# Optimization experiments

Hardware: AMD Instinct MI355X
Metric: run time of the kernel (lower is better)

The kernel has to match this reference:

```python
import jax, jax.numpy as jnp
import numpy as np

N = 3072          # n_vertices
D = 512           # embedding_size (hardcoded in module)
ALPHA = 0.2       # LeakyReLU slope
AVG_DEG = 32
NEG_INF = -9e15
N_ITERS = 10
TRIPLET_MARGIN = 400.0


def setup_inputs() -> dict:
    key = jax.random.key(0)
    ks = jax.random.split(key, 14)
    s = 0.05  # weight init scale
    emb = jax.random.normal(ks[0], (N, D), dtype=jnp.float32) * 0.1
    # symmetric 0/1 adjacency, no self loops, density ~ AVG_DEG/N
    u = jax.random.uniform(ks[1], (N, N))
    A = jnp.triu((u < (AVG_DEG / N)).astype(jnp.float32), 1)
    adj = A + A.T
    rn = lambda k, shp: jax.random.normal(k, shp, dtype=jnp.float32) * s
    return {
        "embeddings": emb,
        "adj": adj,
        "W_n": rn(ks[2], (D, D)), "a_src_n": rn(ks[3], (D,)), "a_dst_n": rn(ks[4], (D,)),
        "W_nn": rn(ks[5], (D, D)), "a_src_nn": rn(ks[6], (D,)), "a_dst_nn": rn(ks[7], (D,)),
        "W_u": rn(ks[8], (2 * D, D)), "b_u": jnp.zeros((D,), dtype=jnp.float32),
        "W_g": rn(ks[9], (D, D)), "a_src_g": rn(ks[10], (D,)), "a_dst_g": rn(ks[11], (D,)),
    }


def _gat_attention(h, adj, W, a_src, a_dst):
    # standard pyGAT layer: Wh = hW; e_ij = LeakyReLU(a_src.Wh_i + a_dst.Wh_j)
    Wh = h @ W                                   # [N, D]
    e = jax.nn.leaky_relu((Wh @ a_src)[:, None] + (Wh @ a_dst)[None, :], ALPHA)
    att = jax.nn.softmax(jnp.where(adj > 0, e, NEG_INF), axis=1)  # [N, N]
    return att, Wh


def reference(embeddings, adj, W_n, a_src_n, a_dst_n, W_nn, a_src_nn, a_dst_nn,
              W_u, b_u, W_g, a_src_g, a_dst_g):
    n = embeddings.shape[0]
    inv_adj = 1.0 - adj - jnp.eye(n, dtype=adj.dtype)  # non-neighbors, no self
    emb = embeddings
    for _ in range(N_ITERS):
        att_n, Wh_n = _gat_attention(emb, adj, W_n, a_src_n, a_dst_n)
        neigh = jax.nn.elu(att_n @ Wh_n)               # concat=True -> ELU
        att_nn, Wh_nn = _gat_attention(emb, inv_adj, W_nn, a_src_nn, a_dst_nn)
        non_neigh = jax.nn.elu(att_nn @ Wh_nn)
        cat = jnp.concatenate([neigh, non_neigh], axis=1)  # [N, 2D]
        emb = jax.nn.relu(emb + cat @ W_u + b_u)
    sq = jnp.sum(emb * emb, axis=1)
    d2 = sq[:, None] + sq[None, :] - 2.0 * (emb @ emb.T)
    dist = jnp.sqrt(jnp.maximum(d2, 1e-12))            # [N, N]
    embedding_loss = jnp.sum(dist * (-adj))
    triplet_loss = jnp.maximum(embedding_loss + TRIPLET_MARGIN, 0.0)
    # glimpse layer returns the attention matrix itself
    att_g, _ = _gat_attention(emb, adj, W_g, a_src_g, a_dst_g)
    confidence = jnp.max(att_g, axis=1)
    log_conf = jnp.mean(jnp.log(confidence + 1e-8) - jnp.log(1e-8))
    return jnp.stack([triplet_loss, embedding_loss, log_conf])
```

## Files before the change

### kernel.cpp

```cpp
#include <hip/hip_runtime.h>
#include <math.h>

#define N_V 3072
#define D_E 512
#define EDGE_CAP 128
constexpr float LRELU_ALPHA = 0.2f;
constexpr float NEG_INF_F = -9e15f;

typedef __attribute__((ext_vector_type(8))) short bf16x8;
typedef __attribute__((ext_vector_type(4))) float f32x4;
typedef __attribute__((ext_vector_type(4))) unsigned short ushort4v;
typedef __attribute__((ext_vector_type(2))) unsigned short ushort2v;

__device__ inline unsigned short f2bf(float f) {
    union { float f; unsigned int u; } x; x.f = f;
    unsigned int r = x.u + 0x7fffu + ((x.u >> 16) & 1u);
    return (unsigned short)(r >> 16);
}
__device__ inline float bf2f(unsigned short b) {
    union { unsigned int u; float f; } x; x.u = ((unsigned int)b) << 16;
    return x.f;
}

__device__ inline void xcd_swizzle(int& bx, int& by) {
    int gx = gridDim.x, nwg = gx * gridDim.y;
    int flat = by * gx + bx;
    int q = nwg >> 3;
    int swz = (flat & 7) * q + (flat >> 3);
    bx = swz % gx; by = swz / gx;
}

template<int EPI>
__global__ __launch_bounds__(256) void gemm_bf16(
    const unsigned short* __restrict__ A,
    const unsigned short* __restrict__ BT,
    int M, int N, int K,
    unsigned short* __restrict__ C0, int ldc0,
    unsigned short* __restrict__ C1,
    const float* __restrict__ addv,
    const float* __restrict__ bias,
    float* __restrict__ Cf)
{
    constexpr int BM = 128, BN = 64, BK = 64;
    __shared__ unsigned short As[BM * BK + BN * BK];
    unsigned short* Bs = As + BM * BK;
    const int tid  = threadIdx.x;
    int bxi = blockIdx.x, byi = blockIdx.y;
    xcd_swizzle(bxi, byi);
    const int bm   = byi * BM, bn = bxi * BN;
    const int lane = tid & 63, wid = tid >> 6;
    const int wr   = wid >> 1, wc = wid & 1;
    const int lr   = lane & 15, lk = lane >> 4;

    f32x4 acc[4][2];
    #pragma unroll
    for (int i = 0; i < 4; ++i)
        #pragma unroll
        for (int j = 0; j < 2; ++j)
            acc[i][j] = (f32x4)(0.f);

    auto asp = (__attribute__((address_space(3))) unsigned short*)As;
    auto bsp = (__attribute__((address_space(3))) unsigned short*)Bs;

    for (int k0 = 0; k0 < K; k0 += BK) {
        #pragma unroll
        for (int l = 0; l < 4; ++l) {
            int li = l * 256 + tid;
            int row = li >> 3, slot = li & 7;
            int gs = slot ^ (row & 7);
            __builtin_amdgcn_global_load_lds(
                (const __attribute__((address_space(1))) void*)(A + (size_t)(bm + row) * K + k0 + gs * 8),
                (__attribute__((address_space(3))) void*)(asp + li * 8), 16, 0, 0);
        }
        #pragma unroll
        for (int l = 0; l < 2; ++l) {
            int li = l * 256 + tid;
            int row = li >> 3, slot = li & 7;
            int gs = slot ^ (row & 7);
            __builtin_amdgcn_global_load_lds(
                (const __attribute__((address_space(1))) void*)(BT + (size_t)(bn + row) * K + k0 + gs * 8),
                (__attribute__((address_space(3))) void*)(bsp + li * 8), 16, 0, 0);
        }
        __syncthreads();

        #pragma unroll
        for (int ks = 0; ks < 2; ++ks) {
            bf16x8 af[4], bfr[2];
            #pragma unroll
            for (int fm = 0; fm < 4; ++fm) {
                int row = wr * 64 + fm * 16 + lr;
                int sl = (ks * 4 + lk) ^ (row & 7);
                af[fm] = *(const bf16x8*)(As + row * BK + sl * 8);
            }
            #pragma unroll
            for (int fn = 0; fn < 2; ++fn) {
                int col = wc * 32 + fn * 16 + lr;
                int sl = (ks * 4 + lk) ^ (col & 7);
                bfr[fn] = *(const bf16x8*)(Bs + col * BK + sl * 8);
            }
            #pragma unroll
            for (int fm = 0; fm < 4; ++fm)
                #pragma unroll
                for (int fn = 0; fn < 2; ++fn)
                    acc[fm][fn] = __builtin_amdgcn_mfma_f32_16x16x32_bf16(
                        af[fm], bfr[fn], acc[fm][fn], 0, 0, 0);
        }
        __syncthreads();
    }

    if (EPI == 2) {
        #pragma unroll
        for (int fm = 0; fm < 4; ++fm) {
            #pragma unroll
            for (int fn = 0; fn < 2; ++fn) {
                int row0 = bm + wr * 64 + fm * 16 + lk * 4;
                int col  = bn + wc * 32 + fn * 16 + lr;
                f32x4 v = acc[fm][fn];
                #pragma unroll
                for (int r = 0; r < 4; ++r) {
                    float x = v[r] + addv[(size_t)(row0 + r) * N + col] + bias[col];
                    x = x > 0.f ? x : 0.f;
                    Cf[(size_t)(row0 + r) * N + col] = x;
                    C0[(size_t)(row0 + r) * ldc0 + col] = f2bf(x);
                }
            }
        }
    } else {
        if (bn < 512) {
            #pragma unroll
            for (int fm = 0; fm < 4; ++fm) {
                #pragma unroll
                for (int fn = 0; fn < 2; ++fn) {
                    int row0 = bm + wr * 64 + fm * 16 + lk * 4;
                    int col  = bn + wc * 32 + fn * 16 + lr;
                    #pragma unroll
                    for (int r = 0; r < 4; ++r)
                        C0[(size_t)(row0 + r) * ldc0 + col] = f2bf(acc[fm][fn][r]);
                }
            }
        } else if (bn < 1024) {
            constexpr int TS = 136;
            unsigned short* Ts = As;
            #pragma unroll
            for (int fm = 0; fm < 4; ++fm) {
                #pragma unroll
                for (int fn = 0; fn < 2; ++fn) {
                    int rloc = wr * 64 + fm * 16 + lk * 4;
                    int lc   = wc * 32 + fn * 16 + lr;
                    ushort4v pk;
                    pk.x = f2bf(acc[fm][fn][0]); pk.y = f2bf(acc[fm][fn][1]);
                    pk.z = f2bf(acc[fm][fn][2]); pk.w = f2bf(acc[fm][fn][3]);
                    *(ushort4v*)(Ts + lc * TS + rloc) = pk;
                }
            }
            __syncthreads();
            for (int idx = tid; idx < 64 * 16; idx += 256) {
                int c = idx >> 4, seg = idx & 15;
                bf16x8 pk = *(const bf16x8*)(Ts + c * TS + seg * 8);
                *(bf16x8*)(C1 + (size_t)(bn - 512 + c) * M + bm + seg * 8) = pk;
            }
        } else {
            #pragma unroll
            for (int fm = 0; fm < 4; ++fm) {
                #pragma unroll
                for (int fn = 0; fn < 2; ++fn) {
                    int row0 = bm + wr * 64 + fm * 16 + lk * 4;
                    int col  = bn + wc * 32 + fn * 16 + lr;
                    if (col >= 1024 && col < 1030) {
                        int v = col - 1024;
                        #pragma unroll
                        for (int r = 0; r < 4; ++r)
                            Cf[(size_t)v * N_V + row0 + r] = acc[fm][fn][r];
                    }
                }
            }
        }
    }
}

__global__ __launch_bounds__(256) void gemm_nn64(
    const unsigned short* __restrict__ A,
    const unsigned short* __restrict__ BT,
    unsigned short* __restrict__ cat)
{
    constexpr int BM = 64, BN = 64, BK = 64, K = N_V;
    __shared__ unsigned short As[BM * BK];
    __shared__ unsigned short Bs[BN * BK];
    const int tid = threadIdx.x;
    int bxi = blockIdx.x, byi = blockIdx.y;
    xcd_swizzle(bxi, byi);
    const int bm = byi * BM, bn = bxi * BN;
    const int lane = tid & 63, wid = tid >> 6;
    const int wr = wid >> 1, wc = wid & 1;
    const int lr = lane & 15, lk = lane >> 4;

    f32x4 acc[2][2];
    #pragma unroll
    for (int i = 0; i < 2; ++i)
        #pragma unroll
        for (int j = 0; j < 2; ++j)
            acc[i][j] = (f32x4)(0.f);

    auto asp = (__attribute__((address_space(3))) unsigned short*)As;
    auto bsp = (__attribute__((address_space(3))) unsigned short*)Bs;

    for (int k0 = 0; k0 < K; k0 += BK) {
        #pragma unroll
        for (int l = 0; l < 2; ++l) {
            int li = l * 256 + tid;
            int row = li >> 3, slot = li & 7;
            int gs = slot ^ (row & 7);
            __builtin_amdgcn_global_load_lds(
                (const __attribute__((address_space(1))) void*)(A + (size_t)(bm + row) * K + k0 + gs * 8),
                (__attribute__((address_space(3))) void*)(asp + li * 8), 16, 0, 0);
        }
        #pragma unroll
        for (int l = 0; l < 2; ++l) {
            int li = l * 256 + tid;
            int row = li >> 3, slot = li & 7;
            int gs = slot ^ (row & 7);
            __builtin_amdgcn_global_load_lds(
                (const __attribute__((address_space(1))) void*)(BT + (size_t)(bn + row) * K + k0 + gs * 8),
                (__attribute__((address_space(3))) void*)(bsp + li * 8), 16, 0, 0);
        }
        __syncthreads();

        #pragma unroll
        for (int ks = 0; ks < 2; ++ks) {
            bf16x8 af[2], bfr[2];
            #pragma unroll
            for (int fm = 0; fm < 2; ++fm) {
                int row = wr * 32 + fm * 16 + lr;
                int sl = (ks * 4 + lk) ^ (row & 7);
                af[fm] = *(const bf16x8*)(As + row * BK + sl * 8);
            }
            #pragma unroll
            for (int fn = 0; fn < 2; ++fn) {
                int col = wc * 32 + fn * 16 + lr;
                int sl = (ks * 4 + lk) ^ (col & 7);
                bfr[fn] = *(const bf16x8*)(Bs + col * BK + sl * 8);
            }
            #pragma unroll
            for (int fm = 0; fm < 2; ++fm)
                #pragma unroll
                for (int fn = 0; fn < 2; ++fn)
                    acc[fm][fn] = __builtin_amdgcn_mfma_f32_16x16x32_bf16(
                        af[fm], bfr[fn], acc[fm][fn], 0, 0, 0);
        }
        __syncthreads();
    }

    #pragma unroll
    for (int fm = 0; fm < 2; ++fm) {
        #pragma unroll
        for (int fn = 0; fn < 2; ++fn) {
            int row0 = bm + wr * 32 + fm * 16 + lk * 4;
            int col  = bn + wc * 32 + fn * 16 + lr;
            #pragma unroll
            for (int r = 0; r < 4; ++r) {
                float x = acc[fm][fn][r];
                x = x > 0.f ? x : (expf(x) - 1.f);
                cat[(size_t)(row0 + r) * (2 * D_E) + D_E + col] = f2bf(x);
            }
        }
    }
}

__global__ __launch_bounds__(256) void convT_f32_bf16(
    const float* __restrict__ W, unsigned short* __restrict__ WT, int K, int Nw)
{
    int k = blockIdx.x * 256 + threadIdx.x;
    int n = blockIdx.y;
    if (k < K) WT[(size_t)n * K + k] = f2bf(W[(size_t)k * Nw + n]);
}

__global__ __launch_bounds__(256) void conv_bf16(
    const float* __restrict__ X, unsigned short* __restrict__ Y, int n)
{
    int i = blockIdx.x * 256 + threadIdx.x;
    if (i < n) Y[i] = f2bf(X[i]);
}

__global__ __launch_bounds__(256) void conv_wv_rows(
    const float* __restrict__ wv, unsigned short* __restrict__ W2Tx)
{
    int k = threadIdx.x + (blockIdx.x & 1) * 256;
    int v = blockIdx.x >> 1;
    W2Tx[(size_t)(1024 + v) * D_E + k] = f2bf(wv[v * D_E + k]);
}

__global__ __launch_bounds__(256) void build_graph(
    const float* __restrict__ adj, int* __restrict__ edges,
    int* __restrict__ deg, unsigned int* __restrict__ bitmask)
{
    const int i = blockIdx.x, t = threadIdx.x;
    __shared__ int cnts[256];
    unsigned int word = 0;
    int c = 0;
    if (t < 96) {
        #pragma unroll
        for (int b = 0; b < 32; ++b) {
            int j = t * 32 + b;
            if (adj[(size_t)i * N_V + j] > 0.f) { word |= (1u << b); ++c; }
        }
    }
    cnts[t] = c;
    __syncthreads();
    for (int o = 1; o < 256; o <<= 1) {
        int add = (t >= o) ? cnts[t - o] : 0;
        __syncthreads();
        cnts[t] += add;
        __syncthreads();
    }
    int base = cnts[t] - c;
    if (t < 96) {
        int k = 0;
        #pragma unroll
        for (int b = 0; b < 32; ++b) {
            if ((word >> b) & 1u) {
                int pos = base + k;
                if (pos < EDGE_CAP) edges[(size_t)i * EDGE_CAP + pos] = t * 32 + b;
                ++k;
            }
        }
        bitmask[(size_t)i * 96 + t] = word;
    }
    if (t == 0) deg[i] = cnts[255] < EDGE_CAP ? cnts[255] : EDGE_CAP;
}

__global__ __launch_bounds__(256) void matvec6(
    const float* __restrict__ W_n, const float* __restrict__ W_nn,
    const float* __restrict__ W_g,
    const float* __restrict__ as_n, const float* __restrict__ ad_n,
    const float* __restrict__ as_nn, const float* __restrict__ ad_nn,
    const float* __restrict__ as_g, const float* __restrict__ ad_g,
    float* __restrict__ wv)
{
    const int wave = threadIdx.x >> 6, lane = threadIdx.x & 63;
    const int r = blockIdx.x * 4 + wave;
    float a0 = 0, a1 = 0, a2 = 0, a3 = 0, a4 = 0, a5 = 0;
    #pragma unroll
    for (int k = 0; k < 8; ++k) {
        int c = lane + k * 64;
        float wn = W_n[(size_t)r * D_E + c];
        float wm = W_nn[(size_t)r * D_E + c];
        float wg = W_g[(size_t)r * D_E + c];
        a0 = fmaf(wn, as_n[c], a0);  a1 = fmaf(wn, ad_n[c], a1);
        a2 = fmaf(wm, as_nn[c], a2); a3 = fmaf(wm, ad_nn[c], a3);
        a4 = fmaf(wg, as_g[c], a4);  a5 = fmaf(wg, ad_g[c], a5);
    }
    #pragma unroll
    for (int off = 32; off; off >>= 1) {
        a0 += __shfl_down(a0, off); a1 += __shfl_down(a1, off);
        a2 += __shfl_down(a2, off); a3 += __shfl_down(a3, off);
        a4 += __shfl_down(a4, off); a5 += __shfl_down(a5, off);
    }
    if (lane == 0) {
        wv[0 * D_E + r] = a0; wv[1 * D_E + r] = a1;
        wv[2 * D_E + r] = a2; wv[3 * D_E + r] = a3;
        wv[4 * D_E + r] = a4; wv[5 * D_E + r] = a5;
    }
}

template<int NV>
__global__ __launch_bounds__(256) void sd_dots(
    const unsigned short* __restrict__ emb, const float* __restrict__ wv,
    float* __restrict__ outs)
{
    const int wave = threadIdx.x >> 6, lane = threadIdx.x & 63;
    const int i = blockIdx.x * 4 + wave;
    float acc[NV];
    #pragma unroll
    for (int v = 0; v < NV; ++v) acc[v] = 0.f;
    #pragma unroll
    for (int k = 0; k < 8; ++k) {
        int c = lane + k * 64;
        float x = bf2f(emb[(size_t)i * D_E + c]);
        #pragma unroll
        for (int v = 0; v < NV; ++v) acc[v] = fmaf(x, wv[v * D_E + c], acc[v]);
    }
    #pragma unroll
    for (int off = 32; off; off >>= 1)
        #pragma unroll
        for (int v = 0; v < NV; ++v) acc[v] += __shfl_down(acc[v], off);
    if (lane == 0)
        #pragma unroll
        for (int v = 0; v < NV; ++v) outs[v * N_V + i] = acc[v];
}

__global__ __launch_bounds__(256) void nn_sm_gather(
    const unsigned int* __restrict__ bitmask,
    const int* __restrict__ edges, const int* __restrict__ deg,
    const float* __restrict__ sd,
    const unsigned short* __restrict__ Whn,
    unsigned short* __restrict__ att, unsigned short* __restrict__ cat)
{
    const int t = threadIdx.x;
    __shared__ float red[256];
    if (blockIdx.x < N_V) {
        const int i = blockIdx.x;
        const float* s = sd + 2 * N_V;
        const float* dvec = sd + 3 * N_V;
        __shared__ unsigned int mrow[96];
        if (t < 96) mrow[t] = bitmask[(size_t)i * 96 + t];
        __syncthreads();
        const float si = s[i];
        const float4* dv4 = (const float4*)dvec;
        float e[3][4];
        float mloc = -3.4e38f;
        #pragma unroll
        for (int l = 0; l < 3; ++l) {
            int jv = t + l * 256;
            float4 d = dv4[jv];
            int j0 = jv * 4;
            unsigned int w = mrow[j0 >> 5];
            #pragma unroll
            for (int c = 0; c < 4; ++c) {
                int j = j0 + c;
                bool keep = (((w >> (j & 31)) & 1u) == 0u) && (j != i);
                float x = si + ((const float*)&d)[c];
                x = x > 0.f ? x : LRELU_ALPHA * x;
                e[l][c] = keep ? x : NEG_INF_F;
                mloc = fmaxf(mloc, e[l][c]);
            }
        }
        red[t] = mloc; __syncthreads();
        for (int o = 128; o; o >>= 1) {
            if (t < o) red[t] = fmaxf(red[t], red[t + o]);
            __syncthreads();
        }
        float m = red[0]; __syncthreads();
        float zloc = 0.f;
        #pragma unroll
        for (int l = 0; l < 3; ++l)
            #pragma unroll
            for (int c = 0; c < 4; ++c) { e[l][c] = expf(e[l][c] - m); zloc += e[l][c]; }
        red[t] = zloc; __syncthreads();
        for (int o = 128; o; o >>= 1) {
            if (t < o) red[t] += red[t + o];
            __syncthreads();
        }
        const float zinv = 1.f / red[0];
        #pragma unroll
        for (int l = 0; l < 3; ++l) {
            int jv = t + l * 256;
            ushort4v p;
            p.x = f2bf(e[l][0] * zinv); p.y = f2bf(e[l][1] * zinv);
            p.z = f2bf(e[l][2] * zinv); p.w = f2bf(e[l][3] * zinv);
            *(ushort4v*)(att + (size_t)i * N_V + (size_t)jv * 4) = p;
        }
    } else {
        const int i = blockIdx.x - N_V;
        const float* s = sd;
        const float* dvec = sd + N_V;
        const int cnt = deg[i];
        __shared__ float p[EDGE_CAP];
        __shared__ int lst[EDGE_CAP];
        float ev = -3.4e38f;
        if (t < cnt) {
            int j = edges[(size_t)i * EDGE_CAP + t];
            lst[t] = j;
            float x = s[i] + dvec[j];
            x = x > 0.f ? x : LRELU_ALPHA * x;
            p[t] = x;
            ev = x;
        }
        red[t] = ev; __syncthreads();
        for (int o = 128; o; o >>= 1) {
            if (t < o) red[t] = fmaxf(red[t], red[t + o]);
            __syncthreads();
        }
        float m = red[0]; __syncthreads();
        float pe = 0.f;
        if (t < cnt) { pe = expf(p[t] - m); p[t] = pe; }
        red[t] = pe; __syncthreads();
        for (int o = 128; o; o >>= 1) {
            if (t < o) red[t] += red[t + o];
            __syncthreads();
        }
        const float zinv = 1.f / red[0];
        float a0 = 0.f, a1 = 0.f;
        for (int e = 0; e < cnt; ++e) {
            int j = lst[e];
            float w = p[e] * zinv;
            ushort2v h = *(const ushort2v*)(Whn + (size_t)j * D_E + t * 2);
            a0 = fmaf(w, bf2f(h.x), a0);
            a1 = fmaf(w, bf2f(h.y), a1);
        }
        a0 = a0 > 0.f ? a0 : (expf(a0) - 1.f);
        a1 = a1 > 0.f ? a1 : (expf(a1) - 1.f);
        ushort2v o2; o2.x = f2bf(a0); o2.y = f2bf(a1);
        *(ushort2v*)(cat + (size_t)i * (2 * D_E) + t * 2) = o2;
    }
}

__global__ __launch_bounds__(256) void colsum(
    const float* __restrict__ emb, float* __restrict__ musum)
{
    const int b = blockIdx.x, t = threadIdx.x;
    float s0 = 0.f, s1 = 0.f;
    for (int r = 0; r < 64; ++r) {
        const float* row = emb + (size_t)(b * 64 + r) * D_E;
        s0 += row[t];
        s1 += row[t + 256];
    }
    atomicAdd(&musum[t], s0);
    atomicAdd(&musum[t + 256], s1);
}

__global__ __launch_bounds__(256) void center_bf16(
    const float* __restrict__ emb, const float* __restrict__ musum,
    unsigned short* __restrict__ embc)
{
    int i = blockIdx.x * 256 + threadIdx.x;
    int c = i & (D_E - 1);
    embc[i] = f2bf(emb[i] - musum[c] * (1.f / N_V));
}

__global__ __launch_bounds__(256) void edge_loss_c(
    const int* __restrict__ edges, const int* __restrict__ deg,
    const unsigned short* __restrict__ embc, float* __restrict__ epart)
{
    __shared__ unsigned short rowi[D_E];
    __shared__ float gsum[16];
    const int i = blockIdx.x, t = threadIdx.x;
    if (t < 64) ((bf16x8*)rowi)[t] = ((const bf16x8*)(embc + (size_t)i * D_E))[t];
    __syncthreads();
    const int g = t >> 4, l = t & 15;
    const int cnt = deg[i];
    float sum = 0.f;
    for (int e = g; e < cnt; e += 16) {
        int j = edges[(size_t)i * EDGE_CAP + e];
        float d2 = 0.f;
        #pragma unroll
        for (int q = 0; q < 4; ++q) {
            int off = q * 128 + l * 8;
            bf16x8 a = *(const bf16x8*)(rowi + off);
            bf16x8 b = *(const bf16x8*)(embc + (size_t)j * D_E + off);
            #pragma unroll
            for (int k = 0; k < 8; ++k) {
                float df = bf2f(((unsigned short*)&a)[k]) -
                           bf2f(((unsigned short*)&b)[k]);
                d2 = fmaf(df, df, d2);
            }
        }
        #pragma unroll
        for (int msk = 1; msk < 16; msk <<= 1) d2 += __shfl_xor(d2, msk);
        if (l == 0) sum += sqrtf(fmaxf(d2, 1e-12f));
    }
    if (l == 0) gsum[g] = sum;
    __syncthreads();
    if (t == 0) {
        float tot = 0.f;
        #pragma unroll
        for (int k = 0; k < 16; ++k) tot += gsum[k];
        epart[i] = tot;
    }
}

__global__ __launch_bounds__(256) void conf_kernel(
    const unsigned int* __restrict__ bitmask, const float* __restrict__ s,
    const float* __restrict__ dvec, float* __restrict__ cpart)
{
    const int i = blockIdx.x, t = threadIdx.x;
    __shared__ unsigned int mrow[96];
    __shared__ float red[256];
    if (t < 96) mrow[t] = bitmask[(size_t)i * 96 + t];
    __syncthreads();
    const float si = s[i];
    const float4* dv4 = (const float4*)dvec;
    float e[3][4];
    float mloc = -3.4e38f;
    #pragma unroll
    for (int l = 0; l < 3; ++l) {
        int jv = t + l * 256;
        float4 d = dv4[jv];
        int j0 = jv * 4;
        unsigned int w = mrow[j0 >> 5];
        #pragma unroll
        for (int c = 0; c < 4; ++c) {
            int j = j0 + c;
            bool keep = ((w >> (j & 31)) & 1u) != 0u;
            float x = si + ((const float*)&d)[c];
            x = x > 0.f ? x : LRELU_ALPHA * x;
            e[l][c] = keep ? x : NEG_INF_F;
            mloc = fmaxf(mloc, e[l][c]);
        }
    }
    red[t] = mloc; __syncthreads();
    for (int o = 128; o; o >>= 1) {
        if (t < o) red[t] = fmaxf(red[t], red[t + o]);
        __syncthreads();
    }
    float m = red[0]; __syncthreads();
    float zloc = 0.f;
    #pragma unroll
    for (int l = 0; l < 3; ++l)
        #pragma unroll
        for (int c = 0; c < 4; ++c) zloc += expf(e[l][c] - m);
    red[t] = zloc; __syncthreads();
    for (int o = 128; o; o >>= 1) {
        if (t < o) red[t] += red[t + o];
        __syncthreads();
    }
    if (t == 0) cpart[i] = logf(1.f / red[0] + 1e-8f);
}

__global__ __launch_bounds__(256) void finalize2(
    const float* __restrict__ epart, const float* __restrict__ cpart,
    float* __restrict__ out)
{
    const int t = threadIdx.x;
    float e = 0.f, c = 0.f;
    #pragma unroll
    for (int k = 0; k < 12; ++k) {
        e += epart[t + k * 256];
        c += cpart[t + k * 256];
    }
    __shared__ float re[256], rc[256];
    re[t] = e; rc[t] = c;
    __syncthreads();
    for (int o = 128; o; o >>= 1) {
        if (t < o) { re[t] += re[t + o]; rc[t] += rc[t + o]; }
        __syncthreads();
    }
    if (t == 0) {
        float loss = -re[0];
        out[0] = fmaxf(loss + 400.f, 0.f);
        out[1] = loss;
        out[2] = rc[0] / (float)N_V - logf(1e-8f);
    }
}

extern "C" void kernel_launch(void* const* d_in, const int* in_sizes, int n_in,
                              void* d_out, int out_size, void* d_ws, size_t ws_size,
                              hipStream_t stream) {
    const float* emb_in   = (const float*)d_in[0];
    const float* adj      = (const float*)d_in[1];
    const float* W_n      = (const float*)d_in[2];
    const float* a_src_n  = (const float*)d_in[3];
    const float* a_dst_n  = (const float*)d_in[4];
    const float* W_nn     = (const float*)d_in[5];
    const float* a_src_nn = (const float*)d_in[6];
    const float* a_dst_nn = (const float*)d_in[7];
    const float* W_u      = (const float*)d_in[8];
    const float* b_u      = (const float*)d_in[9];
    const float* W_g      = (const float*)d_in[10];
    const float* a_src_g  = (const float*)d_in[11];
    const float* a_dst_g  = (const float*)d_in[12];
    float* out = (float*)d_out;

    char* p = (char*)d_ws;
    auto alloc = [&](size_t bytes) { char* r = p; p += (bytes + 255) & ~(size_t)255; return r; };

    unsigned short* att_nn  = (unsigned short*)alloc((size_t)N_V * N_V * 2);
    unsigned short* Whn     = (unsigned short*)alloc((size_t)N_V * D_E * 2);
    unsigned short* WhTnn   = (unsigned short*)alloc((size_t)D_E * N_V * 2);
    unsigned short* cat_bf  = (unsigned short*)alloc((size_t)N_V * 2 * D_E * 2);
    float*          embf[2] = { (float*)alloc((size_t)N_V * D_E * 4),
                                (float*)alloc((size_t)N_V * D_E * 4) };
    unsigned short* embb[2] = { (unsigned short*)alloc((size_t)N_V * D_E * 2),
                                (unsigned short*)alloc((size_t)N_V * D_E * 2) };
    unsigned short* embc    = (unsigned short*)alloc((size_t)N_V * D_E * 2);
    unsigned short* W2Tx    = (unsigned short*)alloc((size_t)1088 * D_E * 2);
    unsigned short* WuT     = (unsigned short*)alloc((size_t)D_E * (2 * D_E) * 2);
    float*          wv      = (float*)alloc(6 * D_E * 4);
    float*          sd      = (float*)alloc(6 * N_V * 4);
    float*          sdg     = (float*)alloc(2 * N_V * 4);
    float*          musum   = (float*)alloc(D_E * 4);
    float*          epart   = (float*)alloc(N_V * 4);
    float*          cpart   = (float*)alloc(N_V * 4);
    int*            edges   = (int*)alloc((size_t)N_V * EDGE_CAP * 4);
    int*            deg     = (int*)alloc(N_V * 4);
    unsigned int*   bitmask = (unsigned int*)alloc((size_t)N_V * 96 * 4);

    dim3 blk(256);

    hipMemsetAsync(W2Tx, 0, (size_t)1088 * D_E * 2, stream);
    convT_f32_bf16<<<dim3(2, D_E), blk, 0, stream>>>(W_n, W2Tx, D_E, D_E);
    convT_f32_bf16<<<dim3(2, D_E), blk, 0, stream>>>(W_nn, W2Tx + (size_t)D_E * D_E, D_E, D_E);
    convT_f32_bf16<<<dim3(4, D_E), blk, 0, stream>>>(W_u, WuT, 2 * D_E, D_E);
    conv_bf16<<<(N_V * D_E) / 256, blk, 0, stream>>>(emb_in, embb[0], N_V * D_E);
    hipMemcpyAsync(embf[0], emb_in, (size_t)N_V * D_E * 4, hipMemcpyDeviceToDevice, stream);
    hipMemsetAsync(musum, 0, D_E * sizeof(float), stream);
    build_graph<<<N_V, blk, 0, stream>>>(adj, edges, deg, bitmask);
    matvec6<<<D_E / 4, blk, 0, stream>>>(W_n, W_nn, W_g, a_src_n, a_dst_n,
                                         a_src_nn, a_dst_nn, a_src_g, a_dst_g, wv);
    conv_wv_rows<<<12, blk, 0, stream>>>(wv, W2Tx);

    dim3 gW2(17, N_V / 128);
    dim3 gG(8, N_V / 128);
    dim3 gNN(D_E / 64, N_V / 64);

    int cur = 0;
    for (int it = 0; it < 10; ++it) {
        int nxt = cur ^ 1;
        gemm_bf16<5><<<gW2, blk, 0, stream>>>(embb[cur], W2Tx, N_V, 1088, D_E,
                                              Whn, D_E, WhTnn, nullptr, nullptr, sd);
        nn_sm_gather<<<2 * N_V, blk, 0, stream>>>(bitmask, edges, deg, sd,
                                                  Whn, att_nn, cat_bf);
        gemm_nn64<<<gNN, blk, 0, stream>>>(att_nn, WhTnn, cat_bf);
        gemm_bf16<2><<<gG, blk, 0, stream>>>(cat_bf, WuT, N_V, D_E, 2 * D_E,
                                             embb[nxt], D_E, nullptr, embf[cur], b_u, embf[nxt]);
        cur = nxt;
    }

    colsum<<<N_V / 64, blk, 0, stream>>>(embf[cur], musum);
    center_bf16<<<(N_V * D_E) / 256, blk, 0, stream>>>(embf[cur], musum, embc);
    edge_loss_c<<<N_V, blk, 0, stream>>>(edges, deg, embc, epart);
    sd_dots<2><<<N_V / 4, blk, 0, stream>>>(embb[cur], wv + 4 * D_E, sdg);
    conf_kernel<<<N_V, blk, 0, stream>>>(bitmask, sdg, sdg + N_V, cpart);

    finalize2<<<1, blk, 0, stream>>>(epart, cpart, out);
}
```

Before: 853.8 us.

## Split-K the dense non-neighbor attention GEMM and use edge-list confidence softmax

The non-neighbor attention GEMM (3072x512, K=3072) now uses 128x64 tiles and splits K into two halves across a z-dimension. Each half writes fp32 partials, and a new elementwise kernel sums them, applies ELU and stores bf16 into the concat buffer. This keeps the same block count while giving each block more MFMA work per loaded B tile. The cost is extra fp32 partial traffic and one more launch per iteration. Separately, the glimpse confidence softmax now runs one wave per row over the sparse edge list instead of a dense 3072-wide masked row, which removes most of that kernel's work.

```diff
diff --git a/kernel.cpp b/kernel.cpp
--- a/kernel.cpp
+++ b/kernel.cpp
@@ -178,25 +178,27 @@
     }
 }
 
-__global__ __launch_bounds__(256) void gemm_nn64(
+__global__ __launch_bounds__(256) void gemm_nn_sk(
     const unsigned short* __restrict__ A,
     const unsigned short* __restrict__ BT,
-    unsigned short* __restrict__ cat)
-{
-    constexpr int BM = 64, BN = 64, BK = 64, K = N_V;
+    float* __restrict__ Cp)
+{
+    constexpr int BM = 128, BN = 64, BK = 64, K = N_V;
     __shared__ unsigned short As[BM * BK];
     __shared__ unsigned short Bs[BN * BK];
-    const int tid = threadIdx.x;
+    const int tid  = threadIdx.x;
     int bxi = blockIdx.x, byi = blockIdx.y;
     xcd_swizzle(bxi, byi);
-    const int bm = byi * BM, bn = bxi * BN;
+    const int bm   = byi * BM, bn = bxi * BN;
+    const int kh   = K >> 1;
+    const int kbeg = blockIdx.z * kh, kend = kbeg + kh;
     const int lane = tid & 63, wid = tid >> 6;
-    const int wr = wid >> 1, wc = wid & 1;
-    const int lr = lane & 15, lk = lane >> 4;
-
-    f32x4 acc[2][2];
-    #pragma unroll
-    for (int i = 0; i < 2; ++i)
+    const int wr   = wid >> 1, wc = wid & 1;
+    const int lr   = lane & 15, lk = lane >> 4;
+
+    f32x4 acc[4][2];
+    #pragma unroll
+    for (int i = 0; i < 4; ++i)
         #pragma unroll
         for (int j = 0; j < 2; ++j)
             acc[i][j] = (f32x4)(0.f);
@@ -204,9 +206,9 @@
     auto asp = (__attribute__((address_space(3))) unsigned short*)As;
     auto bsp = (__attribute__((address_space(3))) unsigned short*)Bs;
 
-    for (int k0 = 0; k0 < K; k0 += BK) {
-        #pragma unroll
-        for (int l = 0; l < 2; ++l) {
+    for (int k0 = kbeg; k0 < kend; k0 += BK) {
+        #pragma unroll
+        for (int l = 0; l < 4; ++l) {
             int li = l * 256 + tid;
             int row = li >> 3, slot = li & 7;
             int gs = slot ^ (row & 7);
@@ -227,10 +229,10 @@
 
         #pragma unroll
         for (int ks = 0; ks < 2; ++ks) {
-            bf16x8 af[2], bfr[2];
-            #pragma unroll
-            for (int fm = 0; fm < 2; ++fm) {
-                int row = wr * 32 + fm * 16 + lr;
+            bf16x8 af[4], bfr[2];
+            #pragma unroll
+            for (int fm = 0; fm < 4; ++fm) {
+                int row = wr * 64 + fm * 16 + lr;
                 int sl = (ks * 4 + lk) ^ (row & 7);
                 af[fm] = *(const bf16x8*)(As + row * BK + sl * 8);
             }
@@ -241,7 +243,7 @@
                 bfr[fn] = *(const bf16x8*)(Bs + col * BK + sl * 8);
             }
             #pragma unroll
-            for (int fm = 0; fm < 2; ++fm)
+            for (int fm = 0; fm < 4; ++fm)
                 #pragma unroll
                 for (int fn = 0; fn < 2; ++fn)
                     acc[fm][fn] = __builtin_amdgcn_mfma_f32_16x16x32_bf16(
@@ -250,20 +252,38 @@
         __syncthreads();
     }
 
-    #pragma unroll
-    for (int fm = 0; fm < 2; ++fm) {
+    float* Cz = Cp + (size_t)blockIdx.z * N_V * D_E;
+    #pragma unroll
+    for (int fm = 0; fm < 4; ++fm) {
         #pragma unroll
         for (int fn = 0; fn < 2; ++fn) {
-            int row0 = bm + wr * 32 + fm * 16 + lk * 4;
+            int row0 = bm + wr * 64 + fm * 16 + lk * 4;
             int col  = bn + wc * 32 + fn * 16 + lr;
             #pragma unroll
-            for (int r = 0; r < 4; ++r) {
-                float x = acc[fm][fn][r];
-                x = x > 0.f ? x : (expf(x) - 1.f);
-                cat[(size_t)(row0 + r) * (2 * D_E) + D_E + col] = f2bf(x);
-            }
-        }
-    }
+            for (int r = 0; r < 4; ++r)
+                Cz[(size_t)(row0 + r) * D_E + col] = acc[fm][fn][r];
+        }
+    }
+}
+
+__global__ __launch_bounds__(256) void elu_combine2(
+    const float* __restrict__ p0, const float* __restrict__ p1,
+    unsigned short* __restrict__ cat)
+{
+    int idx = blockIdx.x * 256 + threadIdx.x;
+    float4 a = ((const float4*)p0)[idx];
+    float4 b = ((const float4*)p1)[idx];
+    int r = idx >> 7;
+    int cc = (idx & 127) * 4;
+    float v[4] = { a.x + b.x, a.y + b.y, a.z + b.z, a.w + b.w };
+    ushort4v o;
+    #pragma unroll
+    for (int q = 0; q < 4; ++q) {
+        float x = v[q];
+        x = x > 0.f ? x : (expf(x) - 1.f);
+        ((unsigned short*)&o)[q] = f2bf(x);
+    }
+    *(ushort4v*)(cat + (size_t)r * (2 * D_E) + D_E + cc) = o;
 }
 
 __global__ __launch_bounds__(256) void convT_f32_bf16(
@@ -558,52 +578,34 @@
     }
 }
 
-__global__ __launch_bounds__(256) void conf_kernel(
-    const unsigned int* __restrict__ bitmask, const float* __restrict__ s,
-    const float* __restrict__ dvec, float* __restrict__ cpart)
-{
-    const int i = blockIdx.x, t = threadIdx.x;
-    __shared__ unsigned int mrow[96];
-    __shared__ float red[256];
-    if (t < 96) mrow[t] = bitmask[(size_t)i * 96 + t];
-    __syncthreads();
+__global__ __launch_bounds__(256) void conf_edge(
+    const int* __restrict__ edges, const int* __restrict__ deg,
+    const float* __restrict__ s, const float* __restrict__ dvec,
+    float* __restrict__ cpart)
+{
+    const int wave = threadIdx.x >> 6, lane = threadIdx.x & 63;
+    const int i = blockIdx.x * 4 + wave;
+    const int cnt = deg[i];
     const float si = s[i];
-    const float4* dv4 = (const float4*)dvec;
-    float e[3][4];
-    float mloc = -3.4e38f;
-    #pragma unroll
-    for (int l = 0; l < 3; ++l) {
-        int jv = t + l * 256;
-        float4 d = dv4[jv];
-        int j0 = jv * 4;
-        unsigned int w = mrow[j0 >> 5];
-        #pragma unroll
-        for (int c = 0; c < 4; ++c) {
-            int j = j0 + c;
-            bool keep = ((w >> (j & 31)) & 1u) != 0u;
-            float x = si + ((const float*)&d)[c];
-            x = x > 0.f ? x : LRELU_ALPHA * x;
-            e[l][c] = keep ? x : NEG_INF_F;
-            mloc = fmaxf(mloc, e[l][c]);
-        }
-    }
-    red[t] = mloc; __syncthreads();
-    for (int o = 128; o; o >>= 1) {
-        if (t < o) red[t] = fmaxf(red[t], red[t + o]);
-        __syncthreads();
-    }
-    float m = red[0]; __syncthreads();
-    float zloc = 0.f;
-    #pragma unroll
-    for (int l = 0; l < 3; ++l)
-        #pragma unroll
-        for (int c = 0; c < 4; ++c) zloc += expf(e[l][c] - m);
-    red[t] = zloc; __syncthreads();
-    for (int o = 128; o; o >>= 1) {
-        if (t < o) red[t] += red[t + o];
-        __syncthreads();
-    }
-    if (t == 0) cpart[i] = logf(1.f / red[0] + 1e-8f);
+    float x0 = -3.4e38f, x1 = -3.4e38f;
+    if (lane < cnt) {
+        int j = edges[(size_t)i * EDGE_CAP + lane];
+        float x = si + dvec[j];
+        x0 = x > 0.f ? x : LRELU_ALPHA * x;
+    }
+    if (lane + 64 < cnt) {
+        int j = edges[(size_t)i * EDGE_CAP + lane + 64];
+        float x = si + dvec[j];
+        x1 = x > 0.f ? x : LRELU_ALPHA * x;
+    }
+    float m = fmaxf(x0, x1);
+    #pragma unroll
+    for (int msk = 32; msk; msk >>= 1) m = fmaxf(m, __shfl_xor(m, msk));
+    float z = (lane < cnt ? expf(x0 - m) : 0.f) +
+              (lane + 64 < cnt ? expf(x1 - m) : 0.f);
+    #pragma unroll
+    for (int msk = 32; msk; msk >>= 1) z += __shfl_xor(z, msk);
+    if (lane == 0) cpart[i] = logf(1.f / z + 1e-8f);
 }
 
 __global__ __launch_bounds__(256) void finalize2(
@@ -654,6 +656,7 @@
     auto alloc = [&](size_t bytes) { char* r = p; p += (bytes + 255) & ~(size_t)255; return r; };
 
     unsigned short* att_nn  = (unsigned short*)alloc((size_t)N_V * N_V * 2);
+    float*          Cp      = (float*)alloc((size_t)2 * N_V * D_E * 4);
     unsigned short* Whn     = (unsigned short*)alloc((size_t)N_V * D_E * 2);
     unsigned short* WhTnn   = (unsigned short*)alloc((size_t)D_E * N_V * 2);
     unsigned short* cat_bf  = (unsigned short*)alloc((size_t)N_V * 2 * D_E * 2);
@@ -690,7 +693,7 @@
 
     dim3 gW2(17, N_V / 128);
     dim3 gG(8, N_V / 128);
-    dim3 gNN(D_E / 64, N_V / 64);
+    dim3 gNN(8, N_V / 128, 2);
 
     int cur = 0;
     for (int it = 0; it < 10; ++it) {
@@ -699,7 +702,9 @@
                                               Whn, D_E, WhTnn, nullptr, nullptr, sd);
         nn_sm_gather<<<2 * N_V, blk, 0, stream>>>(bitmask, edges, deg, sd,
                                                   Whn, att_nn, cat_bf);
-        gemm_nn64<<<gNN, blk, 0, stream>>>(att_nn, WhTnn, cat_bf);
+        gemm_nn_sk<<<gNN, blk, 0, stream>>>(att_nn, WhTnn, Cp);
+        elu_combine2<<<(N_V * D_E) / (4 * 256), blk, 0, stream>>>(
+            Cp, Cp + (size_t)N_V * D_E, cat_bf);
         gemm_bf16<2><<<gG, blk, 0, stream>>>(cat_bf, WuT, N_V, D_E, 2 * D_E,
                                              embb[nxt], D_E, nullptr, embf[cur], b_u, embf[nxt]);
         cur = nxt;
@@ -709,7 +714,7 @@
     center_bf16<<<(N_V * D_E) / 256, blk, 0, stream>>>(embf[cur], musum, embc);
     edge_loss_c<<<N_V, blk, 0, stream>>>(edges, deg, embc, epart);
     sd_dots<2><<<N_V / 4, blk, 0, stream>>>(embb[cur], wv + 4 * D_E, sdg);
-    conf_kernel<<<N_V, blk, 0, stream>>>(bitmask, sdg, sdg + N_V, cpart);
+    conf_edge<<<N_V / 4, blk, 0, stream>>>(edges, deg, sdg, sdg + N_V, cpart);
 
     finalize2<<<1, blk, 0, stream>>>(epart, cpart, out);
 }
```

Result: no change. 838.8 us (-1.8%).
